# Kernel optimization log

Measured on AMD Instinct MI355X. Metric: run time of the kernel, lower is better.

The kernel has to match this reference:

```python
import jax, jax.numpy as jnp
import numpy as np

N = 26000       # total nodes (1040 graphs * 25 joints)
E = 208000      # total edges
G = 1040        # graphs (16 samples * 65 frames)
FRAMES = 65
F_IN = 6
HID = 128
HEADS = 4
NCLS = 7


def setup_inputs() -> dict:
    key = jax.random.key(0)
    ks = jax.random.split(key, 30)

    def nrm(k, shape, s=0.05):
        return jax.random.normal(k, shape, dtype=jnp.float32) * s

    return {
        "x": jax.random.normal(ks[0], (N, F_IN), dtype=jnp.float32),
        "edge_index": jax.random.randint(ks[1], (2, E), 0, N, dtype=jnp.int32),
        "batch": jnp.arange(N, dtype=jnp.int32) // (N // G),  # 25 nodes per graph
        "w1_root": nrm(ks[2], (F_IN, HID)),
        "w1_nei": nrm(ks[3], (F_IN, HID)),
        "b1": nrm(ks[4], (HID,)),
        "wq": nrm(ks[5], (HID, HEADS * HID)),
        "bq": nrm(ks[6], (HEADS * HID,)),
        "wk": nrm(ks[7], (HID, HEADS * HID)),
        "bk": nrm(ks[8], (HEADS * HID,)),
        "wv": nrm(ks[9], (HID, HEADS * HID)),
        "bv": nrm(ks[10], (HEADS * HID,)),
        "wskip": nrm(ks[11], (HID, HEADS * HID)),
        "bskip": nrm(ks[12], (HEADS * HID,)),
        "skip_w": nrm(ks[13], (HID, HEADS * HID)),
        "lin1_w": nrm(ks[14], (HEADS * HID, HID)),
        "lin1_b": nrm(ks[15], (HID,)),
        "l2_root": nrm(ks[16], (HID, HID)),
        "l2_nei": nrm(ks[17], (HID, HID)),
        "l2_b": nrm(ks[18], (HID,)),
        "l3_root": nrm(ks[19], (HID, HID)),
        "l3_nei": nrm(ks[20], (HID, HID)),
        "l3_b": nrm(ks[21], (HID,)),
        "fc_w": nrm(ks[22], (HID, NCLS)),
        "fc_b": nrm(ks[23], (NCLS,)),
    }


def _graph_conv(x, src, dst, w_root, w_nei, b):
    # PyG GraphConv (aggr='add'): W_root x_i + W_nei * sum_{j in N(i)} x_j + b
    agg = jax.ops.segment_sum(x[src], dst, num_segments=N)
    return x @ w_root + agg @ w_nei + b


def _transformer_conv(x, src, dst, wq, bq, wk, bk, wv, bv, wskip, bskip):
    # PyG TransformerConv, concat=True, root_weight=True, beta=False.
    # Dropout on attention is inference-disabled.
    q = (x @ wq + bq).reshape(N, HEADS, HID)
    k = (x @ wk + bk).reshape(N, HEADS, HID)
    v = (x @ wv + bv).reshape(N, HEADS, HID)
    logits = jnp.einsum('ehc,ehc->eh', q[dst], k[src]) / jnp.sqrt(jnp.float32(HID))
    m = jax.ops.segment_max(logits, dst, num_segments=N)          # [N,H]
    a = jnp.exp(logits - m[dst])                                  # [E,H]
    denom = jax.ops.segment_sum(a, dst, num_segments=N)           # [N,H]
    num = jax.ops.segment_sum(a[:, :, None] * v[src], dst, num_segments=N)  # [N,H,C]
    out = num / jnp.where(denom == 0, 1.0, denom)[:, :, None]
    return out.reshape(N, HEADS * HID) + (x @ wskip + bskip)


def reference(x, edge_index, batch,
              w1_root, w1_nei, b1,
              wq, bq, wk, bk, wv, bv, wskip, bskip,
              skip_w, lin1_w, lin1_b,
              l2_root, l2_nei, l2_b,
              l3_root, l3_nei, l3_b,
              fc_w, fc_b):
    src, dst = edge_index[0], edge_index[1]
    h = jax.nn.relu(_graph_conv(x, src, dst, w1_root, w1_nei, b1))
    skip_out = h @ skip_w  # external skip Linear (no bias)
    h = jax.nn.relu(_transformer_conv(h, src, dst, wq, bq, wk, bk, wv, bv, wskip, bskip) + skip_out)
    h = jax.nn.relu(h @ lin1_w + lin1_b)
    for wr, wn, b in ((l2_root, l2_nei, l2_b), (l3_root, l3_nei, l3_b)):
        h = jax.nn.relu(_graph_conv(h, src, dst, wr, wn, b) + h)
    # global_mean_pool over graphs
    sums = jax.ops.segment_sum(h, batch, num_segments=G)
    cnts = jax.ops.segment_sum(jnp.ones((N,), jnp.float32), batch, num_segments=G)
    pooled = sums / jnp.where(cnts == 0, 1.0, cnts)[:, None]      # [G, HID]
    # average over 65 frames per sample, then classify
    z = pooled.reshape(-1, FRAMES, HID).mean(axis=1)              # [G/65, HID]
    return z @ fc_w + fc_b
```

## Files before the change

### kernel.cpp

```cpp
#include <hip/hip_runtime.h>
#include <math.h>

#define NN 26000
#define NE 208000
#define SCAN_CH 26
#define CNT_BLOCKS 813

typedef __attribute__((ext_vector_type(8))) short bf16x8;
typedef __attribute__((ext_vector_type(4))) float f32x4;
typedef __attribute__((ext_vector_type(2))) float f32x2;
typedef unsigned char u8;

__device__ __forceinline__ float bf2f(ushort u){
  union { unsigned int i; float f; } w; w.i = ((unsigned int)u) << 16; return w.f;
}
__device__ __forceinline__ ushort f2bf(float f){
  union { float f; unsigned int i; } w; w.f = f;
  unsigned int u = w.i + 0x7fffu + ((w.i >> 16) & 1u);
  return (ushort)(u >> 16);
}

__global__ void cp_k(const int* __restrict__ dst, int* __restrict__ cnt,
                     const float* __restrict__ wq, const float* __restrict__ wk,
                     const float* __restrict__ wv, const float* __restrict__ bq,
                     const float* __restrict__ wskip, const float* __restrict__ skw,
                     const float* __restrict__ lin1w,
                     const float* __restrict__ l2r, const float* __restrict__ l2n,
                     const float* __restrict__ l3r, const float* __restrict__ l3n,
                     ushort* __restrict__ wbuf, float* __restrict__ bu){
  int b = blockIdx.x, t = threadIdx.x;
  if (b < CNT_BLOCKS){
    int e = b*256 + t;
    if (e < NE) atomicAdd(&cnt[dst[e]], 1);
    return;
  }
  b -= CNT_BLOCKS;
  if (b < 256){
    int idx = b*256 + t;
    int n = idx >> 7, k2 = idx & 127, h = n >> 7, m = n & 127;
    const float* wqr = wq + (size_t)k2*512 + h*128;
    const float* wkr = wk + (size_t)m*512 + h*128;
    float s = 0.f;
    for (int c = 0; c < 128; ++c) s = fmaf(wqr[c], wkr[c], s);
    wbuf[idx] = f2bf(s);
    return;
  }
  b -= 256;
  if (b < 2){
    int n = b*256 + t;
    int h = n >> 7, m = n & 127;
    const float* wkr = wk + (size_t)m*512 + h*128;
    float s = 0.f;
    for (int c = 0; c < 128; ++c) s = fmaf(bq[h*128 + c], wkr[c], s);
    bu[n] = s;
    return;
  }
  b -= 2;
  if (b < 256){
    int idx = b*256 + t;
    int n = idx >> 7, m = idx & 127;
    wbuf[196608 + idx] = f2bf(wv[(size_t)m*512 + n]);
    return;
  }
  b -= 256;
  if (b < 256){
    int idx = b*256 + t;
    int n = idx >> 7, k2 = idx & 127;
    wbuf[65536 + idx] = f2bf(wskip[(size_t)k2*512 + n] + skw[(size_t)k2*512 + n]);
    return;
  }
  b -= 256;
  if (b < 256){
    int idx = b*256 + t;
    int n = idx >> 9, k2 = idx & 511;
    wbuf[131072 + idx] = f2bf(lin1w[(size_t)k2*128 + n]);
    return;
  }
  b -= 256;
  {
    int idx = b*256 + t;
    int sg = idx >> 14, loc = idx & 16383, n = loc >> 7, k2 = loc & 127;
    const float* w = (sg == 0) ? l2r : (sg == 1) ? l2n : (sg == 2) ? l3r : l3n;
    wbuf[262144 + idx] = f2bf(w[(size_t)k2*128 + n]);
  }
}

__global__ __launch_bounds__(1024) void scan_k(int* __restrict__ cnt_cur, int* __restrict__ off){
  int t = threadIdx.x;
  int base = t * SCAN_CH;
  int v[SCAN_CH];
  #pragma unroll
  for (int j = 0; j < SCAN_CH; ++j){
    int idx = base + j;
    v[j] = (idx < NN) ? cnt_cur[idx] : 0;
  }
  int s = 0;
  #pragma unroll
  for (int j = 0; j < SCAN_CH; ++j) s += v[j];
  __shared__ int ls[1024];
  ls[t] = s; __syncthreads();
  for (int ofs = 1; ofs < 1024; ofs <<= 1){
    int u = (t >= ofs) ? ls[t - ofs] : 0;
    __syncthreads();
    ls[t] += u;
    __syncthreads();
  }
  int run = (t == 0) ? 0 : ls[t-1];
  #pragma unroll
  for (int j = 0; j < SCAN_CH; ++j){
    int idx = base + j;
    if (idx < NN){
      off[idx] = run;
      cnt_cur[idx] = run;
      run += v[j];
    }
  }
  if (t == 1023) off[NN] = ls[1023];
}

__global__ void fill_k(const int* __restrict__ src, const int* __restrict__ dst,
                       int* __restrict__ cur, int* __restrict__ csrc, int E){
  int e = blockIdx.x*256 + threadIdx.x;
  if (e < E){
    int p = atomicAdd(&cur[dst[e]], 1);
    csrc[p] = src[e];
  }
}

__global__ __launch_bounds__(256) void layer1_k(
    const float* __restrict__ x, const int* __restrict__ off,
    const int* __restrict__ csrc, const float* __restrict__ w1r,
    const float* __restrict__ w1n, const float* __restrict__ b1,
    ushort* __restrict__ h1, u8* __restrict__ h1f)
{
  __shared__ float aggs[2][6];
  int slot = threadIdx.x >> 7, c = threadIdx.x & 127;
  int i = blockIdx.x*2 + slot;
  if (c < 6){
    float s = 0.f;
    int e1 = off[i+1];
    for (int j = off[i]; j < e1; ++j) s += x[(size_t)csrc[j]*6 + c];
    aggs[slot][c] = s;
  }
  __syncthreads();
  float s = b1[c];
  #pragma unroll
  for (int f = 0; f < 6; ++f){
    s = fmaf(x[i*6+f],    w1r[f*128+c], s);
    s = fmaf(aggs[slot][f], w1n[f*128+c], s);
  }
  float r = fmaxf(s, 0.f);
  h1[(size_t)i*128 + c] = f2bf(r);
  unsigned int pk = __builtin_amdgcn_cvt_pk_fp8_f32(r, r, 0u, false);
  h1f[(size_t)i*128 + c] = (u8)(pk & 0xffu);
}

__global__ __launch_bounds__(256) void us_k(
    const ushort* __restrict__ A, const ushort* __restrict__ wbuf,
    const float* __restrict__ bu, const float* __restrict__ bskip,
    u8* __restrict__ cu, ushort* __restrict__ cs, int M)
{
  __shared__ ushort smem[2*128*72];
  ushort* Asm = smem;
  ushort* Bsm = smem + 128*72;
  int tid  = threadIdx.x;
  int lane = tid & 63;
  int wid  = tid >> 6;
  int wr = wid >> 1, wc = wid & 1;
  int rowbase = blockIdx.y * 128;
  int seg = blockIdx.x >> 2;
  int colloc = (blockIdx.x & 3) * 128;
  const ushort* BT = wbuf + (seg ? 65536 : 0);
  const float* bias = seg ? bskip : bu;
  int lr = lane & 15, lk = (lane >> 4) * 8;

  f32x4 acc[4][4] = {};

  for (int k0 = 0; k0 < 128; k0 += 64){
    #pragma unroll
    for (int i = 0; i < 4; ++i){
      int c = tid + i*256;
      int r = c >> 3, col8 = (c & 7) * 8;
      int row = rowbase + r;
      bf16x8 av = (bf16x8)0;
      if (row < M) av = *reinterpret_cast<const bf16x8*>(A + (size_t)row*128 + k0 + col8);
      *reinterpret_cast<bf16x8*>(&Asm[r*72 + col8]) = av;
      *reinterpret_cast<bf16x8*>(&Bsm[r*72 + col8]) =
          *reinterpret_cast<const bf16x8*>(BT + (size_t)(colloc + r)*128 + k0 + col8);
    }
    __syncthreads();
    #pragma unroll
    for (int ks = 0; ks < 64; ks += 32){
      bf16x8 af[4], bfr[4];
      #pragma unroll
      for (int i = 0; i < 4; ++i)
        af[i] = *reinterpret_cast<const bf16x8*>(&Asm[(wr*64 + i*16 + lr)*72 + ks + lk]);
      #pragma unroll
      for (int j = 0; j < 4; ++j)
        bfr[j] = *reinterpret_cast<const bf16x8*>(&Bsm[(wc*64 + j*16 + lr)*72 + ks + lk]);
      #pragma unroll
      for (int i = 0; i < 4; ++i)
        #pragma unroll
        for (int j = 0; j < 4; ++j)
          acc[i][j] = __builtin_amdgcn_mfma_f32_16x16x32_bf16(af[i], bfr[j], acc[i][j], 0, 0, 0);
    }
    __syncthreads();
  }

  int rq = lane >> 4;
  #pragma unroll
  for (int i = 0; i < 4; ++i)
    #pragma unroll
    for (int r = 0; r < 4; ++r){
      int lrow = wr*64 + i*16 + rq*4 + r;
      #pragma unroll
      for (int j = 0; j < 4; ++j){
        int lcol = wc*64 + j*16 + lr;
        smem[lrow*136 + lcol] = f2bf(acc[i][j][r] + bias[colloc + lcol]);
      }
    }
  __syncthreads();

  if (seg == 0){
    #pragma unroll
    for (int t = tid; t < 2048; t += 256){
      int r = t >> 4, s8 = (t & 15) * 8;
      int row = rowbase + r;
      if (row < M){
        bf16x8 hv = *reinterpret_cast<const bf16x8*>(&smem[r*136 + s8]);
        unsigned int lo = 0, hi = 0;
        lo = __builtin_amdgcn_cvt_pk_fp8_f32(bf2f((ushort)hv[0]), bf2f((ushort)hv[1]), lo, false);
        lo = __builtin_amdgcn_cvt_pk_fp8_f32(bf2f((ushort)hv[2]), bf2f((ushort)hv[3]), lo, true);
        hi = __builtin_amdgcn_cvt_pk_fp8_f32(bf2f((ushort)hv[4]), bf2f((ushort)hv[5]), hi, false);
        hi = __builtin_amdgcn_cvt_pk_fp8_f32(bf2f((ushort)hv[6]), bf2f((ushort)hv[7]), hi, true);
        uint2 o; o.x = lo; o.y = hi;
        *reinterpret_cast<uint2*>(cu + (size_t)row*512 + colloc + s8) = o;
      }
    }
  } else {
    #pragma unroll
    for (int t = tid; t < 2048; t += 256){
      int r = t >> 4, s8 = (t & 15) * 8;
      int row = rowbase + r;
      if (row < M)
        *reinterpret_cast<bf16x8*>(cs + (size_t)row*512 + colloc + s8) =
            *reinterpret_cast<const bf16x8*>(&smem[r*136 + s8]);
    }
  }
}

__global__ __launch_bounds__(256) void attn_k(
    const u8* __restrict__ u, const u8* __restrict__ h1f,
    ushort* __restrict__ aggout, float* __restrict__ beta,
    const int* __restrict__ off, const int* __restrict__ csrc)
{
  int lane = threadIdx.x & 63;
  int i = blockIdx.x*4 + (threadIdx.x >> 6);
  int g = lane >> 4;
  int cb = (lane & 15) * 8;

  uint2 uv = *reinterpret_cast<const uint2*>(u + (size_t)i*512 + g*128 + cb);
  f32x2 u01 = __builtin_amdgcn_cvt_pk_f32_fp8(uv.x, false);
  f32x2 u23 = __builtin_amdgcn_cvt_pk_f32_fp8(uv.x, true);
  f32x2 u45 = __builtin_amdgcn_cvt_pk_f32_fp8(uv.y, false);
  f32x2 u67 = __builtin_amdgcn_cvt_pk_f32_fp8(uv.y, true);
  float uf[8] = {u01[0], u01[1], u23[0], u23[1], u45[0], u45[1], u67[0], u67[1]};

  float d = 0.f, agg[8] = {};
  int e0 = off[i], e1 = off[i+1];
  uint2 hA, hB, hC, hD;
  if (e0     < e1) hA = *reinterpret_cast<const uint2*>(h1f + (size_t)csrc[e0]*128 + cb);
  if (e0 + 1 < e1) hB = *reinterpret_cast<const uint2*>(h1f + (size_t)csrc[e0+1]*128 + cb);
  if (e0 + 2 < e1) hC = *reinterpret_cast<const uint2*>(h1f + (size_t)csrc[e0+2]*128 + cb);
  if (e0 + 3 < e1) hD = *reinterpret_cast<const uint2*>(h1f + (size_t)csrc[e0+3]*128 + cb);

  for (int j = e0; j < e1; ++j){
    uint2 hc = hA; hA = hB; hB = hC; hC = hD;
    if (j + 4 < e1) hD = *reinterpret_cast<const uint2*>(h1f + (size_t)csrc[j+4]*128 + cb);
    f32x2 h01 = __builtin_amdgcn_cvt_pk_f32_fp8(hc.x, false);
    f32x2 h23 = __builtin_amdgcn_cvt_pk_f32_fp8(hc.x, true);
    f32x2 h45 = __builtin_amdgcn_cvt_pk_f32_fp8(hc.y, false);
    f32x2 h67 = __builtin_amdgcn_cvt_pk_f32_fp8(hc.y, true);
    float hj[8] = {h01[0], h01[1], h23[0], h23[1], h45[0], h45[1], h67[0], h67[1]};
    float p = uf[0]*hj[0];
    #pragma unroll
    for (int c = 1; c < 8; ++c) p = fmaf(uf[c], hj[c], p);
    p += __shfl_xor(p, 1);
    p += __shfl_xor(p, 2);
    p += __shfl_xor(p, 4);
    p += __shfl_xor(p, 8);
    float a = __expf(p * 0.08838834764831845f);
    d += a;
    #pragma unroll
    for (int c = 0; c < 8; ++c) agg[c] = fmaf(a, hj[c], agg[c]);
  }
  float inv = (d > 0.f) ? 1.f/d : 0.f;
  bf16x8 o;
  #pragma unroll
  for (int c = 0; c < 8; ++c) o[c] = (short)f2bf(agg[c]*inv);
  *reinterpret_cast<bf16x8*>(aggout + (size_t)i*512 + g*128 + cb) = o;
  if ((lane & 15) == 0) beta[i*4 + g] = (d > 0.f) ? 1.f : 0.f;
}

__global__ __launch_bounds__(256) void vproj_k(
    const ushort* __restrict__ agg, const ushort* __restrict__ vT,
    const float* __restrict__ bv, const float* __restrict__ beta,
    ushort* __restrict__ s_io, int M)
{
  __shared__ ushort smem[2*128*72];
  __shared__ float sbeta[128];
  ushort* Asm = smem;
  ushort* Bsm = smem + 128*72;
  int tid = threadIdx.x;
  int lane = tid & 63, wid = tid >> 6;
  int wr = wid >> 1, wc = wid & 1;
  int seg = blockIdx.x;
  int rowbase = blockIdx.y * 128;
  int lr = lane & 15, lk = (lane >> 4) * 8;
  int rq = lane >> 4;

  if (tid < 128){
    int row = rowbase + tid;
    sbeta[tid] = (row < M) ? beta[row*4 + seg] : 0.f;
  }

  f32x4 acc[4][4] = {};
  for (int k0 = 0; k0 < 128; k0 += 64){
    #pragma unroll
    for (int i = 0; i < 4; ++i){
      int c = tid + i*256;
      int r = c >> 3, col8 = (c & 7) * 8;
      int row = rowbase + r;
      bf16x8 av = (bf16x8)0;
      if (row < M) av = *reinterpret_cast<const bf16x8*>(agg + (size_t)row*512 + seg*128 + k0 + col8);
      *reinterpret_cast<bf16x8*>(&Asm[r*72 + col8]) = av;
      *reinterpret_cast<bf16x8*>(&Bsm[r*72 + col8]) =
          *reinterpret_cast<const bf16x8*>(vT + (size_t)(seg*128 + r)*128 + k0 + col8);
    }
    __syncthreads();
    #pragma unroll
    for (int ks = 0; ks < 64; ks += 32){
      bf16x8 af[4], bfr[4];
      #pragma unroll
      for (int i = 0; i < 4; ++i)
        af[i] = *reinterpret_cast<const bf16x8*>(&Asm[(wr*64 + i*16 + lr)*72 + ks + lk]);
      #pragma unroll
      for (int j = 0; j < 4; ++j)
        bfr[j] = *reinterpret_cast<const bf16x8*>(&Bsm[(wc*64 + j*16 + lr)*72 + ks + lk]);
      #pragma unroll
      for (int i = 0; i < 4; ++i)
        #pragma unroll
        for (int j = 0; j < 4; ++j)
          acc[i][j] = __builtin_amdgcn_mfma_f32_16x16x32_bf16(af[i], bfr[j], acc[i][j], 0, 0, 0);
    }
    __syncthreads();
  }

  #pragma unroll
  for (int i = 0; i < 4; ++i)
    #pragma unroll
    for (int r = 0; r < 4; ++r){
      int lrow = wr*64 + i*16 + rq*4 + r;
      #pragma unroll
      for (int j = 0; j < 4; ++j){
        int lcol = wc*64 + j*16 + lr;
        float v = acc[i][j][r] + bv[seg*128 + lcol] * sbeta[lrow];
        smem[lrow*136 + lcol] = f2bf(v);
      }
    }
  __syncthreads();
  #pragma unroll
  for (int t = tid; t < 2048; t += 256){
    int r = t >> 4, s8 = (t & 15) * 8;
    int row = rowbase + r;
    if (row < M){
      ushort* p = s_io + (size_t)row*512 + seg*128 + s8;
      bf16x8 sv = *reinterpret_cast<const bf16x8*>(p);
      bf16x8 tv = *reinterpret_cast<const bf16x8*>(&smem[r*136 + s8]);
      bf16x8 o;
      #pragma unroll
      for (int q2 = 0; q2 < 8; ++q2)
        o[q2] = (short)f2bf(fmaxf(bf2f((ushort)sv[q2]) + bf2f((ushort)tv[q2]), 0.f));
      *reinterpret_cast<bf16x8*>(p) = o;
    }
  }
}

__global__ __launch_bounds__(256) void bgemm64_k(
    const ushort* __restrict__ A1, int lda1, const ushort* __restrict__ B1T, int K1,
    const float* __restrict__ bias, ushort* __restrict__ C, int M, int N)
{
  __shared__ ushort As[64][72];
  __shared__ ushort Bs[128][72];
  int tid  = threadIdx.x;
  int lane = tid & 63;
  int wid  = tid >> 6;
  int wr = wid >> 1, wc = wid & 1;
  int rowbase = blockIdx.y * 64;
  int colbase = blockIdx.x * 128;
  int lr = lane & 15, lk = (lane >> 4) * 8;

  f32x4 acc[2][4] = {};

  for (int k0 = 0; k0 < K1; k0 += 64){
    #pragma unroll
    for (int i = 0; i < 2; ++i){
      int c = tid + i*256;
      int r = c >> 3, col8 = (c & 7) * 8;
      int row = rowbase + r;
      bf16x8 av = (bf16x8)0;
      if (row < M) av = *reinterpret_cast<const bf16x8*>(A1 + (size_t)row*lda1 + k0 + col8);
      *reinterpret_cast<bf16x8*>(&As[r][col8]) = av;
    }
    #pragma unroll
    for (int i = 0; i < 4; ++i){
      int c = tid + i*256;
      int r = c >> 3, col8 = (c & 7) * 8;
      *reinterpret_cast<bf16x8*>(&Bs[r][col8]) =
          *reinterpret_cast<const bf16x8*>(B1T + (size_t)(colbase + r)*K1 + k0 + col8);
    }
    __syncthreads();
    #pragma unroll
    for (int ks = 0; ks < 64; ks += 32){
      bf16x8 af[2], bfr[4];
      #pragma unroll
      for (int i = 0; i < 2; ++i)
        af[i] = *reinterpret_cast<const bf16x8*>(&As[wr*32 + i*16 + lr][ks + lk]);
      #pragma unroll
      for (int j = 0; j < 4; ++j)
        bfr[j] = *reinterpret_cast<const bf16x8*>(&Bs[wc*64 + j*16 + lr][ks + lk]);
      #pragma unroll
      for (int i = 0; i < 2; ++i)
        #pragma unroll
        for (int j = 0; j < 4; ++j)
          acc[i][j] = __builtin_amdgcn_mfma_f32_16x16x32_bf16(af[i], bfr[j], acc[i][j], 0, 0, 0);
    }
    __syncthreads();
  }

  int rq = lane >> 4;
  #pragma unroll
  for (int i = 0; i < 2; ++i){
    #pragma unroll
    for (int r = 0; r < 4; ++r){
      int row = rowbase + wr*32 + i*16 + rq*4 + r;
      if (row >= M) continue;
      #pragma unroll
      for (int j = 0; j < 4; ++j){
        int col = colbase + wc*64 + j*16 + lr;
        if (col >= N) continue;
        float v = fmaxf(acc[i][j][r] + bias[col], 0.f);
        C[(size_t)row*N + col] = f2bf(v);
      }
    }
  }
}

__global__ __launch_bounds__(256) void gconv_k(
    const ushort* __restrict__ h, const ushort* __restrict__ WrT,
    const ushort* __restrict__ WnT, const float* __restrict__ bias,
    const int* __restrict__ off, const int* __restrict__ csrc,
    ushort* __restrict__ out, int M)
{
  __shared__ ushort As1[64][136];
  __shared__ ushort As2[64][136];
  int tid = threadIdx.x, lane = tid & 63, wid = tid >> 6;
  int wr = wid >> 1, wc = wid & 1;
  int rowbase = blockIdx.x * 64;
  int lr = lane & 15, lk = (lane >> 4) * 8;

  #pragma unroll
  for (int it = 0; it < 4; ++it){
    int c = tid + it*256;
    int r = c >> 4, col8 = (c & 15) * 8;
    int row = rowbase + r;
    bf16x8 av = (bf16x8)0;
    if (row < M) av = *reinterpret_cast<const bf16x8*>(h + (size_t)row*128 + col8);
    *reinterpret_cast<bf16x8*>(&As1[r][col8]) = av;
  }
  {
    int r = tid >> 2, sl = tid & 3;
    int row = rowbase + r;
    float a[32] = {};
    if (row < M){
      int e1 = off[row+1];
      for (int j = off[row]; j < e1; ++j){
        const ushort* hp = h + (size_t)csrc[j]*128 + sl*32;
        #pragma unroll
        for (int u = 0; u < 4; ++u){
          bf16x8 hv = *reinterpret_cast<const bf16x8*>(hp + u*8);
          #pragma unroll
          for (int p = 0; p < 8; ++p) a[u*8+p] += bf2f((ushort)hv[p]);
        }
      }
    }
    #pragma unroll
    for (int u = 0; u < 4; ++u){
      bf16x8 o;
      #pragma unroll
      for (int p = 0; p < 8; ++p) o[p] = (short)f2bf(a[u*8+p]);
      *reinterpret_cast<bf16x8*>(&As2[r][sl*32 + u*8]) = o;
    }
  }
  __syncthreads();

  f32x4 acc[2][4] = {};
  #pragma unroll
  for (int pass = 0; pass < 2; ++pass){
    const ushort* BT = pass ? WnT : WrT;
    #pragma unroll
    for (int kk = 0; kk < 128; kk += 32){
      bf16x8 af[2], bfr[4];
      #pragma unroll
      for (int i = 0; i < 2; ++i)
        af[i] = pass
          ? *reinterpret_cast<const bf16x8*>(&As2[wr*32 + i*16 + lr][kk + lk])
          : *reinterpret_cast<const bf16x8*>(&As1[wr*32 + i*16 + lr][kk + lk]);
      #pragma unroll
      for (int j = 0; j < 4; ++j)
        bfr[j] = *reinterpret_cast<const bf16x8*>(
            BT + (size_t)(wc*64 + j*16 + lr)*128 + kk + lk);
      #pragma unroll
      for (int i = 0; i < 2; ++i)
        #pragma unroll
        for (int j = 0; j < 4; ++j)
          acc[i][j] = __builtin_amdgcn_mfma_f32_16x16x32_bf16(af[i], bfr[j], acc[i][j], 0, 0, 0);
    }
  }

  int rq = lane >> 4;
  #pragma unroll
  for (int i = 0; i < 2; ++i){
    #pragma unroll
    for (int r = 0; r < 4; ++r){
      int lrow = wr*32 + i*16 + rq*4 + r;
      int row = rowbase + lrow;
      if (row >= M) continue;
      #pragma unroll
      for (int j = 0; j < 4; ++j){
        int col = wc*64 + j*16 + lr;
        float v = acc[i][j][r] + bias[col] + bf2f(As1[lrow][col]);
        out[(size_t)row*128 + col] = f2bf(fmaxf(v, 0.f));
      }
    }
  }
}

__global__ __launch_bounds__(256) void fc1_k(const ushort* __restrict__ h,
                                             float* __restrict__ partial){
  int s = blockIdx.x, c0 = blockIdx.y;
  int t = threadIdx.x;
  int c = t & 127, g = t >> 7;
  float sum = 0.f;
  int rend = (c0 + 1) * 125;
  for (int r = c0*125 + g; r < rend; r += 2)
    sum += bf2f(h[((size_t)s*1625 + r)*128 + c]);
  __shared__ float zs[2][128];
  zs[g][c] = sum; __syncthreads();
  if (g == 0) partial[((size_t)s*13 + c0)*128 + c] = zs[0][c] + zs[1][c];
}

__global__ __launch_bounds__(128) void fc2_k(const float* __restrict__ partial,
    const float* __restrict__ fcw, const float* __restrict__ fcb,
    float* __restrict__ out)
{
  int s = blockIdx.x;
  int c = threadIdx.x;
  float z = 0.f;
  #pragma unroll
  for (int p = 0; p < 13; ++p) z += partial[((size_t)s*13 + p)*128 + c];
  __shared__ float zs[128];
  zs[c] = z * (1.0f/1625.0f);
  __syncthreads();
  if (c < 7){
    float o = fcb[c];
    for (int k2 = 0; k2 < 128; ++k2) o = fmaf(zs[k2], fcw[k2*7 + c], o);
    out[s*7 + c] = o;
  }
}

extern "C" void kernel_launch(void* const* d_in, const int* in_sizes, int n_in,
                              void* d_out, int out_size, void* d_ws, size_t ws_size,
                              hipStream_t stream)
{
  const float* x     = (const float*)d_in[0];
  const int*   ei    = (const int*)  d_in[1];
  const float* w1r   = (const float*)d_in[3];
  const float* w1n   = (const float*)d_in[4];
  const float* b1    = (const float*)d_in[5];
  const float* wq    = (const float*)d_in[6];
  const float* bq    = (const float*)d_in[7];
  const float* wk    = (const float*)d_in[8];
  const float* wv    = (const float*)d_in[10];
  const float* bv    = (const float*)d_in[11];
  const float* wskip = (const float*)d_in[12];
  const float* bskip = (const float*)d_in[13];
  const float* skw   = (const float*)d_in[14];
  const float* lin1w = (const float*)d_in[15];
  const float* lin1b = (const float*)d_in[16];
  const float* l2r   = (const float*)d_in[17];
  const float* l2n   = (const float*)d_in[18];
  const float* l2b   = (const float*)d_in[19];
  const float* l3r   = (const float*)d_in[20];
  const float* l3n   = (const float*)d_in[21];
  const float* l3b   = (const float*)d_in[22];
  const float* fcw   = (const float*)d_in[23];
  const float* fcb   = (const float*)d_in[24];
  float* out = (float*)d_out;

  const int* src = ei;
  const int* dst = ei + NE;

  char* base = (char*)d_ws;
  size_t o = 0;
  auto alloc = [&](size_t bytes) -> void* {
    o = (o + 255) & ~(size_t)255;
    void* p = base + o; o += bytes; return p;
  };
  int*    cnt     = (int*)   alloc((size_t)NN*4);
  int*    off     = (int*)   alloc((size_t)(NN+1)*4);
  int*    csrc    = (int*)   alloc((size_t)NE*4);
  float*  partial = (float*) alloc((size_t)16*13*128*4);
  float*  bu      = (float*) alloc((size_t)512*4);
  float*  beta    = (float*) alloc((size_t)NN*4*4);
  ushort* h1      = (ushort*)alloc((size_t)NN*128*2);
  u8*     h1f     = (u8*)    alloc((size_t)NN*128);
  ushort* wbuf    = (ushort*)alloc((size_t)327680*2);
  u8*     bufU8   = (u8*)    alloc((size_t)NN*512);
  ushort* aggbuf  = (ushort*)alloc((size_t)NN*512*2);
  ushort* bufS    = (ushort*)alloc((size_t)NN*512*2);
  ushort* hbuf    = (ushort*)alloc((size_t)NN*256*2);
  (void)ws_size; (void)in_sizes; (void)n_in; (void)out_size;

  const ushort* lin1T = wbuf + 131072;
  const ushort* vT    = wbuf + 196608;
  const ushort* l2rT  = wbuf + 262144;
  const ushort* l2nT  = wbuf + 278528;
  const ushort* l3rT  = wbuf + 294912;
  const ushort* l3nT  = wbuf + 311296;

  ushort* h3 = hbuf;
  ushort* h4 = hbuf + (size_t)NN*128;
  ushort* h5 = bufS;

  hipMemsetAsync(cnt, 0, (size_t)NN*4, stream);
  cp_k<<<CNT_BLOCKS + 256 + 2 + 256 + 256 + 256 + 256, 256, 0, stream>>>(
      dst, cnt, wq, wk, wv, bq, wskip, skw, lin1w, l2r, l2n, l3r, l3n, wbuf, bu);
  scan_k<<<1, 1024, 0, stream>>>(cnt, off);
  fill_k<<<(NE+255)/256, 256, 0, stream>>>(src, dst, cnt, csrc, NE);

  layer1_k<<<NN/2, 256, 0, stream>>>(x, off, csrc, w1r, w1n, b1, h1, h1f);

  {
    dim3 g(8, (NN+127)/128);
    us_k<<<g, 256, 0, stream>>>(h1, wbuf, bu, bskip, bufU8, bufS, NN);
  }

  attn_k<<<NN/4, 256, 0, stream>>>(bufU8, h1f, aggbuf, beta, off, csrc);

  {
    dim3 g(4, (NN+127)/128);
    vproj_k<<<g, 256, 0, stream>>>(aggbuf, vT, bv, beta, bufS, NN);
  }

  {
    dim3 g(1, (NN+63)/64);
    bgemm64_k<<<g, 256, 0, stream>>>(bufS, 512, lin1T, 512, lin1b, h3, NN, 128);
  }

  gconv_k<<<(NN+63)/64, 256, 0, stream>>>(h3, l2rT, l2nT, l2b, off, csrc, h4, NN);
  gconv_k<<<(NN+63)/64, 256, 0, stream>>>(h4, l3rT, l3nT, l3b, off, csrc, h5, NN);

  {
    dim3 g1(16, 13);
    fc1_k<<<g1, 256, 0, stream>>>(h5, partial);
    fc2_k<<<16, 128, 0, stream>>>(partial, fcw, fcb, out);
  }
}
```

Measured before the change: 293.9 us.

## Fuse V projection, skip add and lin1 GEMM; store attention aggregate in fp8

Merges the per-head V projection (with skip add and ReLU) and the lin1 GEMM into one kernel, vl_k. Each block keeps its 64-row tile of the post-ReLU head output in shared memory and accumulates lin1 across the four heads, so the 512-wide bf16 intermediate is never written back to and re-read from global memory. The attention aggregate is also stored as fp8 instead of bf16, halving its write and read traffic. The cost is lower precision on the aggregate, fewer blocks in the fused kernel, and extra block-wide syncs between weight tiles.

```diff
diff --git a/kernel.cpp b/kernel.cpp
--- a/kernel.cpp
+++ b/kernel.cpp
@@ -251,7 +251,7 @@
 
 __global__ __launch_bounds__(256) void attn_k(
     const u8* __restrict__ u, const u8* __restrict__ h1f,
-    ushort* __restrict__ aggout, float* __restrict__ beta,
+    u8* __restrict__ aggf, float* __restrict__ beta,
     const int* __restrict__ off, const int* __restrict__ csrc)
 {
   int lane = threadIdx.x & 63;
@@ -295,165 +295,145 @@
     for (int c = 0; c < 8; ++c) agg[c] = fmaf(a, hj[c], agg[c]);
   }
   float inv = (d > 0.f) ? 1.f/d : 0.f;
-  bf16x8 o;
-  #pragma unroll
-  for (int c = 0; c < 8; ++c) o[c] = (short)f2bf(agg[c]*inv);
-  *reinterpret_cast<bf16x8*>(aggout + (size_t)i*512 + g*128 + cb) = o;
+  unsigned int lo = 0, hi = 0;
+  lo = __builtin_amdgcn_cvt_pk_fp8_f32(agg[0]*inv, agg[1]*inv, lo, false);
+  lo = __builtin_amdgcn_cvt_pk_fp8_f32(agg[2]*inv, agg[3]*inv, lo, true);
+  hi = __builtin_amdgcn_cvt_pk_fp8_f32(agg[4]*inv, agg[5]*inv, hi, false);
+  hi = __builtin_amdgcn_cvt_pk_fp8_f32(agg[6]*inv, agg[7]*inv, hi, true);
+  uint2 o; o.x = lo; o.y = hi;
+  *reinterpret_cast<uint2*>(aggf + (size_t)i*512 + g*128 + cb) = o;
   if ((lane & 15) == 0) beta[i*4 + g] = (d > 0.f) ? 1.f : 0.f;
 }
 
-__global__ __launch_bounds__(256) void vproj_k(
-    const ushort* __restrict__ agg, const ushort* __restrict__ vT,
-    const float* __restrict__ bv, const float* __restrict__ beta,
-    ushort* __restrict__ s_io, int M)
+__global__ __launch_bounds__(256) void vl_k(
+    const u8* __restrict__ aggf, const ushort* __restrict__ vT,
+    const ushort* __restrict__ lin1T, const float* __restrict__ bv,
+    const float* __restrict__ beta, const ushort* __restrict__ s,
+    const float* __restrict__ lin1b, ushort* __restrict__ h3, int M)
 {
-  __shared__ ushort smem[2*128*72];
-  __shared__ float sbeta[128];
-  ushort* Asm = smem;
-  ushort* Bsm = smem + 128*72;
-  int tid = threadIdx.x;
-  int lane = tid & 63, wid = tid >> 6;
+  __shared__ ushort As[64*136];
+  __shared__ ushort Bs[128*72];
+  __shared__ ushort Hs[64*136];
+  __shared__ float sbeta[64*4];
+  int tid = threadIdx.x, lane = tid & 63, wid = tid >> 6;
   int wr = wid >> 1, wc = wid & 1;
-  int seg = blockIdx.x;
-  int rowbase = blockIdx.y * 128;
-  int lr = lane & 15, lk = (lane >> 4) * 8;
-  int rq = lane >> 4;
-
-  if (tid < 128){
-    int row = rowbase + tid;
-    sbeta[tid] = (row < M) ? beta[row*4 + seg] : 0.f;
-  }
-
-  f32x4 acc[4][4] = {};
-  for (int k0 = 0; k0 < 128; k0 += 64){
-    #pragma unroll
-    for (int i = 0; i < 4; ++i){
-      int c = tid + i*256;
-      int r = c >> 3, col8 = (c & 7) * 8;
+  int rowbase = blockIdx.x * 64;
+  int lr = lane & 15, lk = (lane >> 4) * 8, rq = lane >> 4;
+
+  {
+    int r = tid >> 2, h = tid & 3;
+    int row = rowbase + r;
+    sbeta[r*4 + h] = (row < M) ? beta[row*4 + h] : 0.f;
+  }
+
+  f32x4 acc3[2][4] = {};
+
+  for (int h = 0; h < 4; ++h){
+    #pragma unroll
+    for (int it = 0; it < 4; ++it){
+      int c = tid + it*256;
+      int r = c >> 4, col8 = (c & 15) * 8;
       int row = rowbase + r;
       bf16x8 av = (bf16x8)0;
-      if (row < M) av = *reinterpret_cast<const bf16x8*>(agg + (size_t)row*512 + seg*128 + k0 + col8);
-      *reinterpret_cast<bf16x8*>(&Asm[r*72 + col8]) = av;
-      *reinterpret_cast<bf16x8*>(&Bsm[r*72 + col8]) =
-          *reinterpret_cast<const bf16x8*>(vT + (size_t)(seg*128 + r)*128 + k0 + col8);
-    }
-    __syncthreads();
-    #pragma unroll
-    for (int ks = 0; ks < 64; ks += 32){
-      bf16x8 af[4], bfr[4];
-      #pragma unroll
-      for (int i = 0; i < 4; ++i)
-        af[i] = *reinterpret_cast<const bf16x8*>(&Asm[(wr*64 + i*16 + lr)*72 + ks + lk]);
-      #pragma unroll
-      for (int j = 0; j < 4; ++j)
-        bfr[j] = *reinterpret_cast<const bf16x8*>(&Bsm[(wc*64 + j*16 + lr)*72 + ks + lk]);
-      #pragma unroll
-      for (int i = 0; i < 4; ++i)
+      if (row < M){
+        uint2 f8 = *reinterpret_cast<const uint2*>(aggf + (size_t)row*512 + h*128 + col8);
+        f32x2 a01 = __builtin_amdgcn_cvt_pk_f32_fp8(f8.x, false);
+        f32x2 a23 = __builtin_amdgcn_cvt_pk_f32_fp8(f8.x, true);
+        f32x2 a45 = __builtin_amdgcn_cvt_pk_f32_fp8(f8.y, false);
+        f32x2 a67 = __builtin_amdgcn_cvt_pk_f32_fp8(f8.y, true);
+        av[0] = (short)f2bf(a01[0]); av[1] = (short)f2bf(a01[1]);
+        av[2] = (short)f2bf(a23[0]); av[3] = (short)f2bf(a23[1]);
+        av[4] = (short)f2bf(a45[0]); av[5] = (short)f2bf(a45[1]);
+        av[6] = (short)f2bf(a67[0]); av[7] = (short)f2bf(a67[1]);
+      }
+      *reinterpret_cast<bf16x8*>(&As[r*136 + col8]) = av;
+    }
+
+    f32x4 acc1[2][4] = {};
+    #pragma unroll
+    for (int k0 = 0; k0 < 128; k0 += 64){
+      __syncthreads();
+      #pragma unroll
+      for (int it = 0; it < 4; ++it){
+        int c = tid + it*256;
+        int r = c >> 3, col8 = (c & 7) * 8;
+        *reinterpret_cast<bf16x8*>(&Bs[r*72 + col8]) =
+            *reinterpret_cast<const bf16x8*>(vT + (size_t)(h*128 + r)*128 + k0 + col8);
+      }
+      __syncthreads();
+      #pragma unroll
+      for (int ks = 0; ks < 64; ks += 32){
+        bf16x8 af[2], bfr[4];
+        #pragma unroll
+        for (int i = 0; i < 2; ++i)
+          af[i] = *reinterpret_cast<const bf16x8*>(&As[(wr*32 + i*16 + lr)*136 + k0 + ks + lk]);
         #pragma unroll
         for (int j = 0; j < 4; ++j)
-          acc[i][j] = __builtin_amdgcn_mfma_f32_16x16x32_bf16(af[i], bfr[j], acc[i][j], 0, 0, 0);
-    }
-    __syncthreads();
-  }
-
-  #pragma unroll
-  for (int i = 0; i < 4; ++i)
-    #pragma unroll
-    for (int r = 0; r < 4; ++r){
-      int lrow = wr*64 + i*16 + rq*4 + r;
-      #pragma unroll
-      for (int j = 0; j < 4; ++j){
-        int lcol = wc*64 + j*16 + lr;
-        float v = acc[i][j][r] + bv[seg*128 + lcol] * sbeta[lrow];
-        smem[lrow*136 + lcol] = f2bf(v);
-      }
-    }
-  __syncthreads();
-  #pragma unroll
-  for (int t = tid; t < 2048; t += 256){
-    int r = t >> 4, s8 = (t & 15) * 8;
-    int row = rowbase + r;
-    if (row < M){
-      ushort* p = s_io + (size_t)row*512 + seg*128 + s8;
-      bf16x8 sv = *reinterpret_cast<const bf16x8*>(p);
-      bf16x8 tv = *reinterpret_cast<const bf16x8*>(&smem[r*136 + s8]);
-      bf16x8 o;
-      #pragma unroll
-      for (int q2 = 0; q2 < 8; ++q2)
-        o[q2] = (short)f2bf(fmaxf(bf2f((ushort)sv[q2]) + bf2f((ushort)tv[q2]), 0.f));
-      *reinterpret_cast<bf16x8*>(p) = o;
-    }
-  }
-}
-
-__global__ __launch_bounds__(256) void bgemm64_k(
-    const ushort* __restrict__ A1, int lda1, const ushort* __restrict__ B1T, int K1,
-    const float* __restrict__ bias, ushort* __restrict__ C, int M, int N)
-{
-  __shared__ ushort As[64][72];
-  __shared__ ushort Bs[128][72];
-  int tid  = threadIdx.x;
-  int lane = tid & 63;
-  int wid  = tid >> 6;
-  int wr = wid >> 1, wc = wid & 1;
-  int rowbase = blockIdx.y * 64;
-  int colbase = blockIdx.x * 128;
-  int lr = lane & 15, lk = (lane >> 4) * 8;
-
-  f32x4 acc[2][4] = {};
-
-  for (int k0 = 0; k0 < K1; k0 += 64){
-    #pragma unroll
-    for (int i = 0; i < 2; ++i){
-      int c = tid + i*256;
-      int r = c >> 3, col8 = (c & 7) * 8;
-      int row = rowbase + r;
-      bf16x8 av = (bf16x8)0;
-      if (row < M) av = *reinterpret_cast<const bf16x8*>(A1 + (size_t)row*lda1 + k0 + col8);
-      *reinterpret_cast<bf16x8*>(&As[r][col8]) = av;
-    }
-    #pragma unroll
-    for (int i = 0; i < 4; ++i){
-      int c = tid + i*256;
-      int r = c >> 3, col8 = (c & 7) * 8;
-      *reinterpret_cast<bf16x8*>(&Bs[r][col8]) =
-          *reinterpret_cast<const bf16x8*>(B1T + (size_t)(colbase + r)*K1 + k0 + col8);
-    }
-    __syncthreads();
-    #pragma unroll
-    for (int ks = 0; ks < 64; ks += 32){
-      bf16x8 af[2], bfr[4];
-      #pragma unroll
-      for (int i = 0; i < 2; ++i)
-        af[i] = *reinterpret_cast<const bf16x8*>(&As[wr*32 + i*16 + lr][ks + lk]);
-      #pragma unroll
-      for (int j = 0; j < 4; ++j)
-        bfr[j] = *reinterpret_cast<const bf16x8*>(&Bs[wc*64 + j*16 + lr][ks + lk]);
-      #pragma unroll
-      for (int i = 0; i < 2; ++i)
+          bfr[j] = *reinterpret_cast<const bf16x8*>(&Bs[(wc*64 + j*16 + lr)*72 + ks + lk]);
+        #pragma unroll
+        for (int i = 0; i < 2; ++i)
+          #pragma unroll
+          for (int j = 0; j < 4; ++j)
+            acc1[i][j] = __builtin_amdgcn_mfma_f32_16x16x32_bf16(af[i], bfr[j], acc1[i][j], 0, 0, 0);
+      }
+    }
+
+    #pragma unroll
+    for (int i = 0; i < 2; ++i)
+      #pragma unroll
+      for (int r = 0; r < 4; ++r){
+        int lrow = wr*32 + i*16 + rq*4 + r;
+        int row = rowbase + lrow;
+        #pragma unroll
+        for (int j = 0; j < 4; ++j){
+          int lcol = wc*64 + j*16 + lr;
+          float sv = (row < M) ? bf2f(s[(size_t)row*512 + h*128 + lcol]) : 0.f;
+          float v = fmaxf(sv + acc1[i][j][r] + bv[h*128 + lcol]*sbeta[lrow*4 + h], 0.f);
+          Hs[lrow*136 + lcol] = f2bf(v);
+        }
+      }
+
+    #pragma unroll
+    for (int k0 = 0; k0 < 128; k0 += 64){
+      __syncthreads();
+      #pragma unroll
+      for (int it = 0; it < 4; ++it){
+        int c = tid + it*256;
+        int r = c >> 3, col8 = (c & 7) * 8;
+        *reinterpret_cast<bf16x8*>(&Bs[r*72 + col8]) =
+            *reinterpret_cast<const bf16x8*>(lin1T + (size_t)r*512 + h*128 + k0 + col8);
+      }
+      __syncthreads();
+      #pragma unroll
+      for (int ks = 0; ks < 64; ks += 32){
+        bf16x8 af[2], bfr[4];
+        #pragma unroll
+        for (int i = 0; i < 2; ++i)
+          af[i] = *reinterpret_cast<const bf16x8*>(&Hs[(wr*32 + i*16 + lr)*136 + k0 + ks + lk]);
         #pragma unroll
         for (int j = 0; j < 4; ++j)
-          acc[i][j] = __builtin_amdgcn_mfma_f32_16x16x32_bf16(af[i], bfr[j], acc[i][j], 0, 0, 0);
-    }
-    __syncthreads();
-  }
-
-  int rq = lane >> 4;
-  #pragma unroll
-  for (int i = 0; i < 2; ++i){
+          bfr[j] = *reinterpret_cast<const bf16x8*>(&Bs[(wc*64 + j*16 + lr)*72 + ks + lk]);
+        #pragma unroll
+        for (int i = 0; i < 2; ++i)
+          #pragma unroll
+          for (int j = 0; j < 4; ++j)
+            acc3[i][j] = __builtin_amdgcn_mfma_f32_16x16x32_bf16(af[i], bfr[j], acc3[i][j], 0, 0, 0);
+      }
+    }
+  }
+
+  #pragma unroll
+  for (int i = 0; i < 2; ++i)
     #pragma unroll
     for (int r = 0; r < 4; ++r){
       int row = rowbase + wr*32 + i*16 + rq*4 + r;
       if (row >= M) continue;
       #pragma unroll
       for (int j = 0; j < 4; ++j){
-        int col = colbase + wc*64 + j*16 + lr;
-        if (col >= N) continue;
-        float v = fmaxf(acc[i][j][r] + bias[col], 0.f);
-        C[(size_t)row*N + col] = f2bf(v);
-      }
-    }
-  }
+        int col = wc*64 + j*16 + lr;
+        h3[(size_t)row*128 + col] = f2bf(fmaxf(acc3[i][j][r] + lin1b[col], 0.f));
+      }
+    }
 }
 
 __global__ __launch_bounds__(256) void gconv_k(
@@ -627,7 +607,7 @@
   u8*     h1f     = (u8*)    alloc((size_t)NN*128);
   ushort* wbuf    = (ushort*)alloc((size_t)327680*2);
   u8*     bufU8   = (u8*)    alloc((size_t)NN*512);
-  ushort* aggbuf  = (ushort*)alloc((size_t)NN*512*2);
+  u8*     aggf    = (u8*)    alloc((size_t)NN*512);
   ushort* bufS    = (ushort*)alloc((size_t)NN*512*2);
   ushort* hbuf    = (ushort*)alloc((size_t)NN*256*2);
   (void)ws_size; (void)in_sizes; (void)n_in; (void)out_size;
@@ -656,17 +636,9 @@
     us_k<<<g, 256, 0, stream>>>(h1, wbuf, bu, bskip, bufU8, bufS, NN);
   }
 
-  attn_k<<<NN/4, 256, 0, stream>>>(bufU8, h1f, aggbuf, beta, off, csrc);
-
-  {
-    dim3 g(4, (NN+127)/128);
-    vproj_k<<<g, 256, 0, stream>>>(aggbuf, vT, bv, beta, bufS, NN);
-  }
-
-  {
-    dim3 g(1, (NN+63)/64);
-    bgemm64_k<<<g, 256, 0, stream>>>(bufS, 512, lin1T, 512, lin1b, h3, NN, 128);
-  }
+  attn_k<<<NN/4, 256, 0, stream>>>(bufU8, h1f, aggf, beta, off, csrc);
+
+  vl_k<<<(NN+63)/64, 256, 0, stream>>>(aggf, vT, lin1T, bv, beta, bufS, lin1b, h3, NN);
 
   gconv_k<<<(NN+63)/64, 256, 0, stream>>>(h3, l2rT, l2nT, l2b, off, csrc, h4, NN);
   gconv_k<<<(NN+63)/64, 256, 0, stream>>>(h4, l3rT, l3nT, l3b, off, csrc, h5, NN);
```

After: 299.1 us. About the same (+1.7%).
